# Optimization experiments

Measured on AMD Instinct MI355X. Metric: run time of the kernel, lower is better.

Reference implementation:

```python
import jax, jax.numpy as jnp
import numpy as np

B, S, D = 16, 1024, 512   # batch, encoder_seqlen, embed dim
H, U = 512, 512           # attention hidden_dim, out_dim (= LSTM units)
LN_EPS = 1e-3             # keras LayerNormalization default epsilon


def _layer_norm(x, gamma, beta):
    mu = jnp.mean(x, axis=-1, keepdims=True)
    var = jnp.mean(jnp.square(x - mu), axis=-1, keepdims=True)
    return gamma * (x - mu) * jax.lax.rsqrt(var + LN_EPS) + beta


def setup_inputs() -> dict:
    key = jax.random.key(0)
    ks = jax.random.split(key, 9)
    sd = 1.0 / np.sqrt(D)
    return {
        "embeddings": jax.random.normal(ks[0], (B, S, D), jnp.float32),
        "Wq": jax.random.normal(ks[1], (D, H), jnp.float32) * sd,
        "Wk": jax.random.normal(ks[2], (D, H), jnp.float32) * sd,
        "Wv": jax.random.normal(ks[3], (D, H), jnp.float32) * sd,
        "Wo": jax.random.normal(ks[4], (H, U), jnp.float32) * (1.0 / np.sqrt(H)),
        "gamma": jnp.ones((U,), jnp.float32),
        "beta": jnp.zeros((U,), jnp.float32),
        "lstm_kernel": jax.random.normal(ks[5], (U, 4 * U), jnp.float32) * sd,       # input kernel [D,4U], gate order i,f,c,o
        "lstm_rec_kernel": jax.random.normal(ks[6], (U, 4 * U), jnp.float32) * sd,   # recurrent kernel [U,4U]
        "lstm_bias": jnp.zeros((4 * U,), jnp.float32),
    }


def _attention(x, Wq, Wk, Wv, Wo):
    q = jnp.einsum("bsd,dh->bsh", x, Wq)
    k = jnp.einsum("bsd,dh->bsh", x, Wk)
    v = jnp.einsum("bsd,dh->bsh", x, Wv)
    scores = jnp.einsum("bqh,bkh->bqk", q, k) / jnp.sqrt(jnp.asarray(H, x.dtype))
    attn = jax.nn.softmax(scores, axis=-1)
    return jnp.einsum("bqk,bkh->bqh", attn, v) @ Wo


def _lstm_relu(x, kernel, rec_kernel, bias):
    # keras LSTM with activation='relu', recurrent_activation='sigmoid', return_sequences
    xp = jnp.einsum("bsd,dg->bsg", x, kernel) + bias          # [B,S,4U]
    xp = jnp.swapaxes(xp, 0, 1)                                # [S,B,4U]

    def step(carry, xt):
        h, c = carry
        z = xt + h @ rec_kernel
        i, f, g, o = jnp.split(z, 4, axis=-1)
        i, f, o = jax.nn.sigmoid(i), jax.nn.sigmoid(f), jax.nn.sigmoid(o)
        c = f * c + i * jax.nn.relu(g)
        h = o * jax.nn.relu(c)
        return (h, c), h

    h0 = jnp.zeros((x.shape[0], U), x.dtype)
    _, hs = jax.lax.scan(step, (h0, h0), xp)
    return jnp.swapaxes(hs, 0, 1)                              # [B,S,U]


def reference(embeddings, Wq, Wk, Wv, Wo, gamma, beta, lstm_kernel, lstm_rec_kernel, lstm_bias):
    out = _attention(embeddings, Wq, Wk, Wv, Wo)
    out = _layer_norm(out + embeddings, gamma, beta)           # shared LN params (same layer used twice)
    res = out
    out = _lstm_relu(out, lstm_kernel, lstm_rec_kernel, lstm_bias)
    out = _layer_norm(out + res, gamma, beta)
    return out
```

## Files before the change

kernel.cpp:

```cpp
#include <hip/hip_runtime.h>

typedef unsigned short u16;
typedef unsigned int   u32;
typedef unsigned long long ull;
typedef __attribute__((ext_vector_type(8))) __bf16 bf16x8;
typedef __attribute__((ext_vector_type(4))) float  f32x4;

#define DEV static __device__ __forceinline__

DEV u16 f2bf(float f) {
    u32 u = __float_as_uint(f);
    u = (u + 0x7fffu + ((u >> 16) & 1u)) >> 16;
    return (u16)u;
}
DEV float bf2f(u16 b) { return __uint_as_float(((u32)b) << 16); }
DEV bf16x8 ldfrag(const u16* p) { return *reinterpret_cast<const bf16x8*>(p); }

__global__ __launch_bounds__(256) void k_cvt(const float* __restrict__ in, u16* __restrict__ out, int n) {
    int i = (blockIdx.x * 256 + threadIdx.x) * 4;
    if (i < n) {
        float4 v = *reinterpret_cast<const float4*>(in + i);
        ushort4 o; o.x = f2bf(v.x); o.y = f2bf(v.y); o.z = f2bf(v.z); o.w = f2bf(v.w);
        *reinterpret_cast<ushort4*>(out + i) = o;
    }
}

__global__ __launch_bounds__(256) void k_tr_f2b(const float* __restrict__ in, u16* __restrict__ out,
                                                int R, int C) {
    __shared__ float t[32][33];
    int c0 = blockIdx.x * 32, r0 = blockIdx.y * 32;
    int tx = threadIdx.x % 32, ty = threadIdx.x / 32;
    for (int i = 0; i < 32; i += 8)
        t[ty + i][tx] = in[(r0 + ty + i) * C + c0 + tx];
    __syncthreads();
    for (int i = 0; i < 32; i += 8)
        out[(size_t)(c0 + ty + i) * R + r0 + tx] = f2bf(t[tx][ty + i]);
}

__global__ __launch_bounds__(256) void k_tr_v(const u16* __restrict__ qkv, u16* __restrict__ vt) {
    __shared__ u16 t[32][33];
    int b = blockIdx.z;
    int s0 = blockIdx.x * 32, h0 = blockIdx.y * 32;
    int tx = threadIdx.x % 32, ty = threadIdx.x / 32;
    for (int i = 0; i < 32; i += 8)
        t[ty + i][tx] = qkv[(size_t)(b * 1024 + s0 + ty + i) * 1536 + 1024 + h0 + tx];
    __syncthreads();
    for (int i = 0; i < 32; i += 8)
        vt[(size_t)b * 512 * 1024 + (size_t)(h0 + ty + i) * 1024 + s0 + tx] = t[tx][ty + i];
}

__global__ __launch_bounds__(256) void k_gemm(const u16* __restrict__ A, const u16* __restrict__ Bt,
                                              u16* __restrict__ Cb, const float* __restrict__ bias,
                                              int M, int N, int K, int ldc, int xp_mode) {
    int mtiles = M >> 7;
    int mt = blockIdx.x % mtiles, nt = blockIdx.x / mtiles;
    int m0 = mt << 7, n0 = nt << 7;
    int lane = threadIdx.x & 63, wid = threadIdx.x >> 6;
    int wm = (wid >> 1) * 64, wn = (wid & 1) * 64;
    int ls = lane & 15, g = lane >> 4;
    f32x4 acc[4][4] = {};
    const u16* Ap = A + (size_t)(m0 + wm + ls) * K + g * 8;
    const u16* Bp = Bt + (size_t)(n0 + wn + ls) * K + g * 8;
    for (int k0 = 0; k0 < K; k0 += 32) {
        bf16x8 a[4], b[4];
        #pragma unroll
        for (int i = 0; i < 4; i++) a[i] = ldfrag(Ap + (size_t)i * 16 * K + k0);
        #pragma unroll
        for (int j = 0; j < 4; j++) b[j] = ldfrag(Bp + (size_t)j * 16 * K + k0);
        #pragma unroll
        for (int i = 0; i < 4; i++)
            #pragma unroll
            for (int j = 0; j < 4; j++)
                acc[i][j] = __builtin_amdgcn_mfma_f32_16x16x32_bf16(a[i], b[j], acc[i][j], 0, 0, 0);
    }
    #pragma unroll
    for (int i = 0; i < 4; i++)
        #pragma unroll
        for (int j = 0; j < 4; j++) {
            int col = n0 + wn + j * 16 + ls;
            float bv = bias ? bias[col] : 0.f;
            #pragma unroll
            for (int r = 0; r < 4; r++) {
                int row = m0 + wm + i * 16 + g * 4 + r;
                u16 val = f2bf(acc[i][j][r] + bv);
                if (xp_mode) {
                    int b_ = row >> 10, s_ = row & 1023;
                    int gate = col >> 9, u = col & 511;
                    int jj = u >> 5, uu = u & 31;
                    Cb[(((size_t)jj * 1024 + s_) * 16 + b_) * 128 + gate * 32 + uu] = val;
                } else {
                    Cb[(size_t)row * ldc + col] = val;
                }
            }
        }
}

__global__ __launch_bounds__(256) void k_attn(const u16* __restrict__ qkv, const u16* __restrict__ vt,
                                              u16* __restrict__ attnO) {
    __shared__ u16 P[16 * 1024];
    __shared__ float mbuf[4][16], lbuf[4][16];
    int b = blockIdx.x >> 6, qt = blockIdx.x & 63;
    int q0 = qt * 16;
    int lane = threadIdx.x & 63, w = threadIdx.x >> 6;
    int ls = lane & 15, g = lane >> 4;
    const float sc = 0.04419417382f;

    f32x4 acc[16] = {};
    const u16* Qp = qkv + (size_t)(b * 1024 + q0 + ls) * 1536 + g * 8;
    const u16* Kp = qkv + (size_t)(b * 1024 + w * 256 + ls) * 1536 + 512 + g * 8;
    for (int k0 = 0; k0 < 512; k0 += 32) {
        bf16x8 a = ldfrag(Qp + k0);
        #pragma unroll
        for (int f = 0; f < 16; f++) {
            bf16x8 bb = ldfrag(Kp + (size_t)f * 16 * 1536 + k0);
            acc[f] = __builtin_amdgcn_mfma_f32_16x16x32_bf16(a, bb, acc[f], 0, 0, 0);
        }
    }
    float mx[4] = {-1e30f, -1e30f, -1e30f, -1e30f};
    #pragma unroll
    for (int f = 0; f < 16; f++)
        #pragma unroll
        for (int r = 0; r < 4; r++) mx[r] = fmaxf(mx[r], acc[f][r]);
    #pragma unroll
    for (int d = 1; d < 16; d <<= 1)
        #pragma unroll
        for (int r = 0; r < 4; r++) mx[r] = fmaxf(mx[r], __shfl_xor(mx[r], d, 64));
    if (ls == 0)
        #pragma unroll
        for (int r = 0; r < 4; r++) mbuf[w][g * 4 + r] = mx[r];
    __syncthreads();
    float m[4];
    #pragma unroll
    for (int r = 0; r < 4; r++) {
        int row = g * 4 + r;
        m[r] = fmaxf(fmaxf(mbuf[0][row], mbuf[1][row]), fmaxf(mbuf[2][row], mbuf[3][row])) * sc;
    }
    float sum[4] = {0.f, 0.f, 0.f, 0.f};
    #pragma unroll
    for (int f = 0; f < 16; f++)
        #pragma unroll
        for (int r = 0; r < 4; r++) {
            int row = g * 4 + r, col = w * 256 + f * 16 + ls;
            float e = __expf(acc[f][r] * sc - m[r]);
            sum[r] += e;
            P[(row * 1024 + col) ^ ((row & 7) << 3)] = f2bf(e);
        }
    #pragma unroll
    for (int d = 1; d < 16; d <<= 1)
        #pragma unroll
        for (int r = 0; r < 4; r++) sum[r] += __shfl_xor(sum[r], d, 64);
    if (ls == 0)
        #pragma unroll
        for (int r = 0; r < 4; r++) lbuf[w][g * 4 + r] = sum[r];
    __syncthreads();

    f32x4 o[8] = {};
    const bf16x8* Pv = reinterpret_cast<const bf16x8*>(P);
    const u16* Vp = vt + (size_t)b * 512 * 1024 + (size_t)(w * 128 + ls) * 1024 + g * 8;
    for (int k0 = 0; k0 < 1024; k0 += 32) {
        bf16x8 a = Pv[(ls * 128 + (k0 >> 3) + g) ^ (ls & 7)];
        #pragma unroll
        for (int q = 0; q < 8; q++) {
            bf16x8 bb = ldfrag(Vp + (size_t)q * 16 * 1024 + k0);
            o[q] = __builtin_amdgcn_mfma_f32_16x16x32_bf16(a, bb, o[q], 0, 0, 0);
        }
    }
    #pragma unroll
    for (int q = 0; q < 8; q++) {
        int col = w * 128 + q * 16 + ls;
        #pragma unroll
        for (int r = 0; r < 4; r++) {
            int row = g * 4 + r;
            float l = lbuf[0][row] + lbuf[1][row] + lbuf[2][row] + lbuf[3][row];
            attnO[(size_t)(b * 1024 + q0 + row) * 512 + col] = f2bf(o[q][r] / l);
        }
    }
}

__global__ __launch_bounds__(256) void k_projln(const u16* __restrict__ attnO, const u16* __restrict__ WoT,
                                                const float* __restrict__ emb, const float* __restrict__ gamma,
                                                const float* __restrict__ beta, float* __restrict__ out1f,
                                                u16* __restrict__ out1b) {
    __shared__ float buf[16][512];
    int m0 = blockIdx.x * 16;
    int lane = threadIdx.x & 63, w = threadIdx.x >> 6;
    int ls = lane & 15, g = lane >> 4;
    f32x4 acc[8] = {};
    const u16* Ap = attnO + (size_t)(m0 + ls) * 512 + g * 8;
    const u16* Bp = WoT + (size_t)(w * 128 + ls) * 512 + g * 8;
    for (int k0 = 0; k0 < 512; k0 += 32) {
        bf16x8 a = ldfrag(Ap + k0);
        #pragma unroll
        for (int q = 0; q < 8; q++) {
            bf16x8 bb = ldfrag(Bp + (size_t)q * 16 * 512 + k0);
            acc[q] = __builtin_amdgcn_mfma_f32_16x16x32_bf16(a, bb, acc[q], 0, 0, 0);
        }
    }
    #pragma unroll
    for (int q = 0; q < 8; q++) {
        int col = w * 128 + q * 16 + ls;
        #pragma unroll
        for (int r = 0; r < 4; r++) {
            int row = g * 4 + r;
            buf[row][col] = acc[q][r] + emb[(size_t)(m0 + row) * 512 + col];
        }
    }
    __syncthreads();
    int row = threadIdx.x >> 4, c0 = threadIdx.x & 15;
    float s = 0.f, s2 = 0.f;
    for (int c = c0; c < 512; c += 16) { float x = buf[row][c]; s += x; s2 += x * x; }
    #pragma unroll
    for (int d = 1; d < 16; d <<= 1) { s += __shfl_xor(s, d, 64); s2 += __shfl_xor(s2, d, 64); }
    float mu = s * (1.f / 512.f);
    float var = s2 * (1.f / 512.f) - mu * mu;
    float rs = rsqrtf(var + 1e-3f);
    for (int c = c0; c < 512; c += 16) {
        float y = gamma[c] * (buf[row][c] - mu) * rs + beta[c];
        out1f[(size_t)(m0 + row) * 512 + c] = y;
        out1b[(size_t)(m0 + row) * 512 + c] = f2bf(y);
    }
}

__global__ __launch_bounds__(256) void k_init2(ull* hbuf) {
    int i = blockIdx.x * 256 + threadIdx.x;
    if (i < 8192) hbuf[i] = 0ull;
}

__global__ __launch_bounds__(256) void k_lstm(const u16* __restrict__ xpp, const u16* __restrict__ rT,
                                              ull* hbuf , float* __restrict__ hseq) {
    int j = blockIdx.x;
    int tid = threadIdx.x;
    int lane = tid & 63, w = tid >> 6;
    int ls = lane & 15, g = lane >> 4;
    __shared__ float z[16][132];
    __shared__ u16 hb[8192];
    __shared__ u16 xb[2][2048];
    u32* hb32 = (u32*)hb;

    bf16x8 rf[2][16];
    {
        const u16* Bp = rT + (size_t)(w * 512 + j * 32 + ls) * 512 + g * 8;
        #pragma unroll
        for (int q = 0; q < 2; q++)
            #pragma unroll
            for (int kk = 0; kk < 16; kk++)
                rf[q][kk] = ldfrag(Bp + (size_t)q * 16 * 512 + kk * 32);
    }
    float cA = 0.f, cB = 0.f;

    for (int i = tid; i < 4096; i += 256) hb32[i] = 0;
    {
        uint4 v = *reinterpret_cast<const uint4*>(xpp + ((size_t)j * 1024) * 2048 + tid * 8);
        *reinterpret_cast<uint4*>(&xb[0][tid * 8]) = v;
    }
    __syncthreads();

    int bb_ = tid >> 4, uu0 = (tid & 15) * 2;
    int eprod = bb_ * 256 + j * 16 + (uu0 >> 1);

    for (int s = 0; s < 1024; s++) {
        uint4 nx;
        if (s + 1 < 1024)
            nx = *reinterpret_cast<const uint4*>(xpp + ((size_t)j * 1024 + s + 1) * 2048 + tid * 8);

        f32x4 acc[2] = {};
        #pragma unroll
        for (int kk = 0; kk < 16; kk++) {
            int aidx = (ls * 512 + kk * 32 + g * 8) ^ ((ls & 7) << 3);
            bf16x8 a = ldfrag(&hb[aidx]);
            acc[0] = __builtin_amdgcn_mfma_f32_16x16x32_bf16(a, rf[0][kk], acc[0], 0, 0, 0);
            acc[1] = __builtin_amdgcn_mfma_f32_16x16x32_bf16(a, rf[1][kk], acc[1], 0, 0, 0);
        }
        #pragma unroll
        for (int q = 0; q < 2; q++)
            #pragma unroll
            for (int r = 0; r < 4; r++)
                z[g * 4 + r][w * 32 + q * 16 + ls] = acc[q][r];
        __syncthreads();

        float hres0, hres1;
        {
            const u16* xr = &xb[s & 1][bb_ * 128];
            #pragma unroll
            for (int p = 0; p < 2; p++) {
                int uu = uu0 + p;
                float zi = z[bb_][uu]      + bf2f(xr[uu]);
                float zf = z[bb_][32 + uu] + bf2f(xr[32 + uu]);
                float zg = z[bb_][64 + uu] + bf2f(xr[64 + uu]);
                float zo = z[bb_][96 + uu] + bf2f(xr[96 + uu]);
                float ii = 1.f / (1.f + __expf(-zi));
                float ff = 1.f / (1.f + __expf(-zf));
                float gg = fmaxf(zg, 0.f);
                float oo = 1.f / (1.f + __expf(-zo));
                float cp = p ? cB : cA;
                float cn = ff * cp + ii * gg;
                if (p) cB = cn; else cA = cn;
                float h = oo * fmaxf(cn, 0.f);
                if (p) hres1 = h; else hres0 = h;
            }
        }

        if (s + 1 < 1024) {
            ull pk = ((ull)((u32)f2bf(hres0) | ((u32)f2bf(hres1) << 16)) << 32) | (u32)(s + 1);
            __hip_atomic_store(hbuf + ((s + 1) & 1) * 4096 + eprod, pk,
                               __ATOMIC_RELAXED, __HIP_MEMORY_SCOPE_AGENT);
        }
        *reinterpret_cast<float2*>(&hseq[((size_t)bb_ * 1024 + s) * 512 + j * 32 + uu0]) =
            make_float2(hres0, hres1);
        if (s + 1 < 1024)
            *reinterpret_cast<uint4*>(&xb[(s + 1) & 1][tid * 8]) = nx;

        if (s + 1 < 1024) {
            const ull* src = hbuf + ((s + 1) & 1) * 4096;
            u32 want = (u32)(s + 1);
            ull v[16];
            #pragma unroll
            for (int i = 0; i < 16; i++)
                v[i] = __hip_atomic_load(src + i * 256 + tid,
                                         __ATOMIC_RELAXED, __HIP_MEMORY_SCOPE_AGENT);
            u32 stale = 0;
            #pragma unroll
            for (int i = 0; i < 16; i++)
                stale |= (u32)((u32)v[i] != want) << i;
            while (stale) {
                __builtin_amdgcn_s_sleep(1);
                #pragma unroll
                for (int i = 0; i < 16; i++)
                    if (stale & (1u << i))
                        v[i] = __hip_atomic_load(src + i * 256 + tid,
                                                 __ATOMIC_RELAXED, __HIP_MEMORY_SCOPE_AGENT);
                u32 ns = 0;
                #pragma unroll
                for (int i = 0; i < 16; i++)
                    ns |= (u32)((u32)v[i] != want) << i;
                stale = ns;
            }
            __syncthreads();
            #pragma unroll
            for (int i = 0; i < 16; i++) {
                int e = i * 256 + tid;
                int b = e >> 8, up = e & 255;
                hb32[(b * 256 + up) ^ ((b & 7) << 2)] = (u32)(v[i] >> 32);
            }
            __syncthreads();
        }
    }
}

__global__ __launch_bounds__(256) void k_finln(float* __restrict__ io, const float* __restrict__ res,
                                               const float* __restrict__ gamma, const float* __restrict__ beta) {
    int m0 = blockIdx.x * 16;
    int row = threadIdx.x >> 4, c0 = threadIdx.x & 15;
    size_t base = (size_t)(m0 + row) * 512;
    float x[32];
    float s = 0.f, s2 = 0.f;
    #pragma unroll
    for (int i = 0; i < 32; i++) {
        int cc = c0 + i * 16;
        x[i] = io[base + cc] + res[base + cc];
        s += x[i]; s2 += x[i] * x[i];
    }
    #pragma unroll
    for (int d = 1; d < 16; d <<= 1) { s += __shfl_xor(s, d, 64); s2 += __shfl_xor(s2, d, 64); }
    float mu = s * (1.f / 512.f);
    float var = s2 * (1.f / 512.f) - mu * mu;
    float rs = rsqrtf(var + 1e-3f);
    #pragma unroll
    for (int i = 0; i < 32; i++) {
        int cc = c0 + i * 16;
        io[base + cc] = gamma[cc] * (x[i] - mu) * rs + beta[cc];
    }
}

extern "C" void kernel_launch(void* const* d_in, const int* in_sizes, int n_in,
                              void* d_out, int out_size, void* d_ws, size_t ws_size,
                              hipStream_t stream) {
    (void)in_sizes; (void)n_in; (void)out_size; (void)ws_size;
    const float* emb   = (const float*)d_in[0];
    const float* Wq    = (const float*)d_in[1];
    const float* Wk    = (const float*)d_in[2];
    const float* Wv    = (const float*)d_in[3];
    const float* Wo    = (const float*)d_in[4];
    const float* gamma = (const float*)d_in[5];
    const float* beta  = (const float*)d_in[6];
    const float* lk    = (const float*)d_in[7];
    const float* lr    = (const float*)d_in[8];
    const float* lb    = (const float*)d_in[9];

    char* w = (char*)d_ws;
    size_t o = 0;
    u16* WqkvT = (u16*)(w + o); o += (size_t)1536 * 512 * 2;
    u16* WoT   = (u16*)(w + o); o += (size_t)512 * 512 * 2;
    u16* kT    = (u16*)(w + o); o += (size_t)2048 * 512 * 2;
    u16* rT    = (u16*)(w + o); o += (size_t)2048 * 512 * 2;
    u16* Xbf   = (u16*)(w + o); o += (size_t)16384 * 512 * 2;
    u16* QKV   = (u16*)(w + o); o += (size_t)16384 * 1536 * 2;
    u16* Vt    = (u16*)(w + o); o += (size_t)16 * 512 * 1024 * 2;
    float* out1f = (float*)(w + o); o += (size_t)16384 * 512 * 4;
    u16* out1b = (u16*)(w + o); o += (size_t)16384 * 512 * 2;
    ull* hbuf  = (ull*)(w + o);  o += (size_t)2 * 4096 * 8;
    u16* attnO = Xbf;
    u16* xpp   = QKV;
    float* outp = (float*)d_out;

    k_cvt<<<8192, 256, 0, stream>>>(emb, Xbf, 16384 * 512);
    k_tr_f2b<<<dim3(16, 16), 256, 0, stream>>>(Wq, WqkvT, 512, 512);
    k_tr_f2b<<<dim3(16, 16), 256, 0, stream>>>(Wk, WqkvT + 512 * 512, 512, 512);
    k_tr_f2b<<<dim3(16, 16), 256, 0, stream>>>(Wv, WqkvT + 1024 * 512, 512, 512);
    k_tr_f2b<<<dim3(16, 16), 256, 0, stream>>>(Wo, WoT, 512, 512);
    k_tr_f2b<<<dim3(64, 16), 256, 0, stream>>>(lk, kT, 512, 2048);
    k_tr_f2b<<<dim3(64, 16), 256, 0, stream>>>(lr, rT, 512, 2048);
    k_gemm<<<128 * 12, 256, 0, stream>>>(Xbf, WqkvT, QKV, nullptr, 16384, 1536, 512, 1536, 0);
    k_tr_v<<<dim3(32, 16, 16), 256, 0, stream>>>(QKV, Vt);
    k_attn<<<1024, 256, 0, stream>>>(QKV, Vt, attnO);
    k_projln<<<1024, 256, 0, stream>>>(attnO, WoT, emb, gamma, beta, out1f, out1b);
    k_gemm<<<128 * 16, 256, 0, stream>>>(out1b, kT, xpp, lb, 16384, 2048, 512, 2048, 1);
    k_init2<<<32, 256, 0, stream>>>(hbuf);
    k_lstm<<<16, 256, 0, stream>>>(xpp, rT, hbuf, outp);
    k_finln<<<1024, 256, 0, stream>>>(outp, out1f, gamma, beta);
}
```

Before: 3.420 ms.

## Stage GEMM tiles in LDS via direct global-to-LDS loads with swizzle

The GEMM kernel now cooperatively loads 128x32 A and B tiles into shared memory with global_load_lds and an XOR swizzle. Waves then read MFMA fragments from LDS, so data is reused across waves instead of each wave issuing redundant global loads. There is no double buffering, so each k-step waits on the loads and adds two barriers. A barrier is also removed in the recurrent kernel before its LDS h-buffer write, which saves sync cost per step but may create a read/write race.

```diff
diff --git a/kernel.cpp b/kernel.cpp
--- a/kernel.cpp
+++ b/kernel.cpp
@@ -58,20 +58,47 @@
     int lane = threadIdx.x & 63, wid = threadIdx.x >> 6;
     int wm = (wid >> 1) * 64, wn = (wid & 1) * 64;
     int ls = lane & 15, g = lane >> 4;
+    __shared__ u16 As[128 * 32], Bs[128 * 32];
     f32x4 acc[4][4] = {};
-    const u16* Ap = A + (size_t)(m0 + wm + ls) * K + g * 8;
-    const u16* Bp = Bt + (size_t)(n0 + wn + ls) * K + g * 8;
+
+    int srow[2], soff[2];
+    #pragma unroll
+    for (int t = 0; t < 2; t++) {
+        int r16 = t * 4 + wid;
+        srow[t] = r16 * 16 + (lane >> 2);
+        soff[t] = ((lane & 3) ^ ((srow[t] >> 1) & 3)) * 8;
+    }
+
     for (int k0 = 0; k0 < K; k0 += 32) {
+        #pragma unroll
+        for (int t = 0; t < 2; t++) {
+            int r16 = t * 4 + wid;
+            __builtin_amdgcn_global_load_lds(
+                (const __attribute__((address_space(1))) void*)(A + (size_t)(m0 + srow[t]) * K + k0 + soff[t]),
+                (__attribute__((address_space(3))) void*)(As + r16 * 512), 16, 0, 0);
+            __builtin_amdgcn_global_load_lds(
+                (const __attribute__((address_space(1))) void*)(Bt + (size_t)(n0 + srow[t]) * K + k0 + soff[t]),
+                (__attribute__((address_space(3))) void*)(Bs + r16 * 512), 16, 0, 0);
+        }
+        asm volatile("s_waitcnt vmcnt(0)" ::: "memory");
+        __syncthreads();
         bf16x8 a[4], b[4];
         #pragma unroll
-        for (int i = 0; i < 4; i++) a[i] = ldfrag(Ap + (size_t)i * 16 * K + k0);
-        #pragma unroll
-        for (int j = 0; j < 4; j++) b[j] = ldfrag(Bp + (size_t)j * 16 * K + k0);
+        for (int i = 0; i < 4; i++) {
+            int row = wm + i * 16 + ls;
+            a[i] = ldfrag(&As[row * 32 + (g ^ ((row >> 1) & 3)) * 8]);
+        }
+        #pragma unroll
+        for (int j = 0; j < 4; j++) {
+            int row = wn + j * 16 + ls;
+            b[j] = ldfrag(&Bs[row * 32 + (g ^ ((row >> 1) & 3)) * 8]);
+        }
         #pragma unroll
         for (int i = 0; i < 4; i++)
             #pragma unroll
             for (int j = 0; j < 4; j++)
                 acc[i][j] = __builtin_amdgcn_mfma_f32_16x16x32_bf16(a[i], b[j], acc[i][j], 0, 0, 0);
+        __syncthreads();
     }
     #pragma unroll
     for (int i = 0; i < 4; i++)
@@ -335,7 +362,6 @@
                     ns |= (u32)((u32)v[i] != want) << i;
                 stale = ns;
             }
-            __syncthreads();
             #pragma unroll
             for (int i = 0; i < 16; i++) {
                 int e = i * 256 + tid;
```

Result: faster. 3.268 ms (-4.4%).
